# Performance work log

Hardware: AMD Instinct MI355X
Metric: run time of the kernel (lower is better)

## Reference

```python
import jax, jax.numpy as jnp
import numpy as np

H_DIM = 1024


def setup_inputs() -> dict:
    key = jax.random.key(0)
    k1, k2, k3, k4 = jax.random.split(key, 4)
    B, S, H = 8, 2048, H_DIM
    scale = 1.0 / np.sqrt(H)
    x = jax.random.normal(k1, (B, S, H), dtype=jnp.float32)
    attention_mask = jnp.ones((B, S), dtype=jnp.int32)
    wq = jax.random.normal(k2, (H, H), dtype=jnp.float32) * scale
    wk = jax.random.normal(k3, (H, H), dtype=jnp.float32) * scale
    wv = jax.random.normal(k4, (H, H), dtype=jnp.float32) * scale
    return {"x": x, "attention_mask": attention_mask, "wq": wq, "wk": wk, "wv": wv}


def reference(x, attention_mask, wq, wk, wv):
    # x: [B,S,H]; torch Linear(no bias): y = x @ W.T
    B, S, H = x.shape
    q = jnp.einsum('bsh,oh->bso', x, wq)
    k = jnp.einsum('bsh,oh->bso', x, wk)
    v = jnp.einsum('bsh,oh->bso', x, wv)
    qk = jnp.einsum('bqh,bkh->bqk', q, k) / jnp.sqrt(jnp.asarray(H, jnp.float32))
    # causal: mask positions where key index > query index (strict upper triangle)
    causal = jnp.triu(jnp.ones((S, S), dtype=bool), k=1)  # [S,S]
    m = attention_mask.astype(bool)                        # [B,S]
    allowed = m[:, None, :] & m[:, :, None]                # d & e: key-valid AND query-valid
    condition = causal[None, :, :] | jnp.logical_not(allowed)
    qk = jnp.where(condition, -jnp.inf, qk)
    att = jax.nn.softmax(qk, axis=-1)
    att = jnp.where(jnp.isnan(att), 0.0, att)  # fully-masked rows -> 0
    return jnp.einsum('bqk,bkh->bqh', att, v)
```

## Files before the change

kernel.cpp:

```cpp
#include <hip/hip_runtime.h>
#include <stdint.h>

typedef unsigned short u16;
typedef __bf16 bf16x8 __attribute__((ext_vector_type(8)));
typedef float f32x4 __attribute__((ext_vector_type(4)));
typedef u16 ushort8 __attribute__((ext_vector_type(8)));

#define SB 8
#define SS 2048
#define SH 1024
#define MTOT (SB*SS)
#define LOG2E 1.44269504088896f
#define SEXP (1.44269504088896f/32.f)

typedef __attribute__((address_space(3))) void lds_void;
typedef __attribute__((address_space(1))) const void gbl_void;

__device__ __forceinline__ float bf2f(u16 v) {
    union { unsigned int u; float f; } x; x.u = ((unsigned int)v) << 16; return x.f;
}
__device__ __forceinline__ u16 f2bf(float f) {
    unsigned int u = __builtin_bit_cast(unsigned int, f);
    u += 0x7fffu + ((u >> 16) & 1u);
    return (u16)(u >> 16);
}

__global__ void cvt_all(const float* __restrict__ x,  const float* __restrict__ wq,
                        const float* __restrict__ wk, const float* __restrict__ wv,
                        u16* __restrict__ xb, u16* __restrict__ wb) {
    const int NX = MTOT * SH / 8, NW = SH * SH / 8;
    int i = blockIdx.x * 256 + threadIdx.x;
    const float* src; u16* dst; int off;
    if (i < NX)               { src = x;  dst = xb;                        off = i; }
    else if (i < NX + NW)     { src = wq; dst = wb;                        off = i - NX; }
    else if (i < NX + 2 * NW) { src = wk; dst = wb + (size_t)SH * SH;      off = i - NX - NW; }
    else                      { src = wv; dst = wb + (size_t)2 * SH * SH;  off = i - NX - 2 * NW; }
    const float4* p = (const float4*)(src + (size_t)off * 8);
    float4 a = p[0], b = p[1];
    ushort8 r;
    r[0] = f2bf(a.x); r[1] = f2bf(a.y); r[2] = f2bf(a.z); r[3] = f2bf(a.w);
    r[4] = f2bf(b.x); r[5] = f2bf(b.y); r[6] = f2bf(b.z); r[7] = f2bf(b.w);
    *(ushort8*)(dst + (size_t)off * 8) = r;
}

__device__ __forceinline__ void stage_tile(const u16* __restrict__ g, int ld,
                                           u16* lds, int w, int l) {
#pragma unroll
    for (int i = 0; i < 4; i++) {
        int chunk = i * 4 + w;
        int r = chunk * 8 + (l >> 3);
        int c = (l & 7) * 8;
        __builtin_amdgcn_global_load_lds(
            (gbl_void*)(g + (size_t)r * ld + c),
            (lds_void*)(lds + chunk * 512), 16, 0, 0);
    }
}

__device__ __forceinline__ void mfma_tile(const u16* As, const u16* Bs,
                                          f32x4 acc[4][4], int w, int l) {
    int wr = (w >> 1) * 64, wc = (w & 1) * 64;
    int lr = l & 15, lk = (l >> 4) * 8;
#pragma unroll
    for (int kk = 0; kk < 2; kk++) {
        bf16x8 af[4], bb[4];
#pragma unroll
        for (int m = 0; m < 4; m++)
            af[m] = *(const bf16x8*)(const void*)(As + (wr + m * 16 + lr) * 64 + kk * 32 + lk);
#pragma unroll
        for (int n = 0; n < 4; n++)
            bb[n] = *(const bf16x8*)(const void*)(Bs + (wc + n * 16 + lr) * 64 + kk * 32 + lk);
#pragma unroll
        for (int m = 0; m < 4; m++)
#pragma unroll
            for (int n = 0; n < 4; n++)
                acc[m][n] = __builtin_amdgcn_mfma_f32_16x16x32_bf16(af[m], bb[n], acc[m][n], 0, 0, 0);
    }
}

#define QNT 16

#define STAGE8(gbase, ld, bufidx, h, t) do {                                          \
    const u16* _g = (gbase) + ((size_t)((h)*128 + srow)) * (ld) + (size_t)(t)*64 + scol; \
    u16* _d = &lds4[bufidx][((h)*128 + (w << 3)) * 64];                               \
    __builtin_amdgcn_global_load_lds((gbl_void*)_g, (lds_void*)_d, 16, 0, 0);         \
    __builtin_amdgcn_global_load_lds((gbl_void*)(_g + (size_t)64*(ld)),               \
                                     (lds_void*)(_d + 64*64), 16, 0, 0);              \
} while (0)

#define LDA8(mf, kkv) (*(const bf16x8*)(const void*)(Ab + (wr + (mf)*16 + rrow)*64 + rk##kkv))
#define LDB8(nf, kkv) (*(const bf16x8*)(const void*)(Bb + (wc + (nf)*16 + rrow)*64 + rk##kkv))

#define MFMA_PAIR(mf, A0, A1)                                                          \
    acc[mf][0] = __builtin_amdgcn_mfma_f32_16x16x32_bf16(A0, b00, acc[mf][0], 0,0,0);  \
    acc[mf][0] = __builtin_amdgcn_mfma_f32_16x16x32_bf16(A1, b01, acc[mf][0], 0,0,0);  \
    acc[mf][1] = __builtin_amdgcn_mfma_f32_16x16x32_bf16(A0, b10, acc[mf][1], 0,0,0);  \
    acc[mf][1] = __builtin_amdgcn_mfma_f32_16x16x32_bf16(A1, b11, acc[mf][1], 0,0,0);  \
    acc[mf][2] = __builtin_amdgcn_mfma_f32_16x16x32_bf16(A0, b20, acc[mf][2], 0,0,0);  \
    acc[mf][2] = __builtin_amdgcn_mfma_f32_16x16x32_bf16(A1, b21, acc[mf][2], 0,0,0);  \
    acc[mf][3] = __builtin_amdgcn_mfma_f32_16x16x32_bf16(A0, b30, acc[mf][3], 0,0,0);  \
    acc[mf][3] = __builtin_amdgcn_mfma_f32_16x16x32_bf16(A1, b31, acc[mf][3], 0,0,0);

#define PH_BAR_MID()                       \
    __builtin_amdgcn_sched_barrier(0);     \
    __builtin_amdgcn_s_barrier();          \
    __builtin_amdgcn_sched_barrier(0);

#define PH_BAR_END()                       \
    __builtin_amdgcn_sched_barrier(0);     \
    __builtin_amdgcn_s_barrier();          \
    __builtin_amdgcn_sched_barrier(0);

__global__ __launch_bounds__(512, 2) void gemm_qkv8(
    const u16* __restrict__ X, const u16* __restrict__ W,
    u16* __restrict__ Q, u16* __restrict__ Kd, u16* __restrict__ Vd) {
    __shared__ u16 lds4[4][256 * 64];

    int tid = threadIdx.x, w = tid >> 6, l = tid & 63;
    int bid = blockIdx.x;
    int wg = (bid & 7) * 96 + (bid >> 3);
    int mt = wg / 12, nb = wg % 12;

    const u16* gA = X + (size_t)mt * 256 * SH;
    const u16* gB = W + (size_t)nb * 256 * SH;

    int srow = (w << 3) + (l >> 3);
    int scol = (((l & 7) ^ ((l >> 3) & 7)) << 3);
    int wr = (w >> 2) * 128, wc = (w & 3) * 64;
    int rrow = l & 15;
    int rk0 = (((l >> 4) ^ (l & 7)) << 3);
    int rk1 = (((4 + (l >> 4)) ^ (l & 7)) << 3);

    f32x4 acc[8][4];
#pragma unroll
    for (int m = 0; m < 8; m++)
#pragma unroll
        for (int n = 0; n < 4; n++) acc[m][n] = (f32x4){0.f, 0.f, 0.f, 0.f};

    STAGE8(gA, SH, 0, 0, 0); STAGE8(gA, SH, 0, 1, 0);
    STAGE8(gB, SH, 2, 0, 0); STAGE8(gB, SH, 2, 1, 0);
    STAGE8(gB, SH, 3, 0, 1); STAGE8(gB, SH, 3, 1, 1);
    asm volatile("s_waitcnt vmcnt(4)" ::: "memory");
    __builtin_amdgcn_s_barrier();
    __builtin_amdgcn_sched_barrier(0);

    for (int t = 0; t < QNT; ++t) {
        const int p = t & 1;
        const u16* Ab = &lds4[p][0];
        const u16* Bb = &lds4[2 + p][0];

        bf16x8 b00 = LDB8(0, 0), b01 = LDB8(0, 1), b10 = LDB8(1, 0), b11 = LDB8(1, 1);
        bf16x8 b20 = LDB8(2, 0), b21 = LDB8(2, 1), b30 = LDB8(3, 0), b31 = LDB8(3, 1);
        {
            bf16x8 a00 = LDA8(0, 0), a01 = LDA8(0, 1), a10 = LDA8(1, 0), a11 = LDA8(1, 1);
            bf16x8 a20 = LDA8(2, 0), a21 = LDA8(2, 1), a30 = LDA8(3, 0), a31 = LDA8(3, 1);
            if (t + 1 < QNT) { STAGE8(gA, SH, (t + 1) & 1, 0, t + 1); STAGE8(gA, SH, (t + 1) & 1, 1, t + 1); }
            PH_BAR_MID();
            __builtin_amdgcn_s_setprio(1);
            MFMA_PAIR(0, a00, a01);
            MFMA_PAIR(1, a10, a11);
            MFMA_PAIR(2, a20, a21);
            MFMA_PAIR(3, a30, a31);
            __builtin_amdgcn_s_setprio(0);
            PH_BAR_END();
        }
        {
            bf16x8 a00 = LDA8(4, 0), a01 = LDA8(4, 1), a10 = LDA8(5, 0), a11 = LDA8(5, 1);
            bf16x8 a20 = LDA8(6, 0), a21 = LDA8(6, 1), a30 = LDA8(7, 0), a31 = LDA8(7, 1);
            if (t + 2 < QNT) { STAGE8(gB, SH, 2 + (t & 1), 0, t + 2); STAGE8(gB, SH, 2 + (t & 1), 1, t + 2); }
            if (t + 2 < QNT)      asm volatile("s_waitcnt vmcnt(4)" ::: "memory");
            else if (t + 1 < QNT) asm volatile("s_waitcnt vmcnt(0)" ::: "memory");
            PH_BAR_MID();
            __builtin_amdgcn_s_setprio(1);
            MFMA_PAIR(4, a00, a01);
            MFMA_PAIR(5, a10, a11);
            MFMA_PAIR(6, a20, a21);
            MFMA_PAIR(7, a30, a31);
            __builtin_amdgcn_s_setprio(0);
            PH_BAR_END();
        }
    }

    u16* outp = (nb < 4 ? Q : (nb < 8 ? Kd : Vd));
    size_t colb = (size_t)(nb & 3) * 256;
    int g = l >> 4, c = l & 15;
    u16* S = &lds4[0][0];
    __syncthreads();
#pragma unroll
    for (int pass = 0; pass < 2; ++pass) {
        if ((w >> 2) == pass) {
#pragma unroll
            for (int mf = 0; mf < 8; mf++)
#pragma unroll
                for (int j = 0; j < 4; j++) {
                    int rl = mf * 16 + g * 4 + j;
#pragma unroll
                    for (int nf = 0; nf < 4; nf++)
                        S[rl * 264 + wc + nf * 16 + c] = f2bf(acc[mf][nf][j]);
                }
        }
        __syncthreads();
#pragma unroll
        for (int q8 = 0; q8 < 8; ++q8) {
            int idx = q8 * 4096 + tid * 8;
            int row = idx >> 8;
            int colu = idx & 255;
            *(ushort8*)(outp + ((size_t)(mt * 256 + pass * 128 + row)) * SH + colb + colu)
                = *(const ushort8*)(S + row * 264 + colu);
        }
        __syncthreads();
    }
}

__global__ void transpose_v(const u16* __restrict__ V, u16* __restrict__ Vt) {
    __shared__ u16 t[64][80];
    int s0 = blockIdx.x * 64, o0 = blockIdx.y * 64, b = blockIdx.z;
    const u16* src = V + (size_t)b * SS * SH;
    u16* dst = Vt + (size_t)b * SH * SS;
    int tid = threadIdx.x;
#pragma unroll
    for (int it = 0; it < 2; it++) {
        int idx = it * 256 + tid;
        int r = idx >> 3, gq = idx & 7;
        *(ushort8*)&t[r][gq * 8] = *(const ushort8*)&src[(size_t)(s0 + r) * SH + o0 + gq * 8];
    }
    __syncthreads();
#pragma unroll
    for (int it = 0; it < 2; it++) {
        int idx = it * 256 + tid;
        int rr = idx >> 3, cc = idx & 7;
        ushort8 v;
#pragma unroll
        for (int e = 0; e < 8; e++) v[e] = t[cc * 8 + e][rr];
        *(ushort8*)&dst[(size_t)(o0 + rr) * SS + s0 + cc * 8] = v;
    }
}

__global__ __launch_bounds__(256, 2) void gemm_scores(
    const u16* __restrict__ Q, const u16* __restrict__ K,
    u16* __restrict__ P, float* __restrict__ lb,
    const int* __restrict__ amask) {
    __shared__ u16 As[128 * 64];
    __shared__ u16 Bs[128 * 64];
    int tid = threadIdx.x, w = tid >> 6, l = tid & 63;
    int x = blockIdx.x;
    int wk_ = (x & 7) * 136 + (x >> 3);
    int b = wk_ / 136, t = wk_ % 136;
    int qt = (int)((sqrtf(8.f * (float)t + 1.f) - 1.f) * 0.5f);
    while ((qt + 1) * (qt + 2) / 2 <= t) qt++;
    while (qt * (qt + 1) / 2 > t) qt--;
    int kt = t - qt * (qt + 1) / 2;
    const u16* A = Q + ((size_t)b * SS + (size_t)qt * 128) * SH;
    const u16* Bt = K + ((size_t)b * SS + (size_t)kt * 128) * SH;
    f32x4 acc[4][4];
#pragma unroll
    for (int m = 0; m < 4; m++)
#pragma unroll
        for (int n = 0; n < 4; n++) acc[m][n] = (f32x4){0.f, 0.f, 0.f, 0.f};
    for (int k0 = 0; k0 < SH; k0 += 64) {
        stage_tile(A + k0, SH, As, w, l);
        stage_tile(Bt + k0, SH, Bs, w, l);
        __syncthreads();
        mfma_tile(As, Bs, acc, w, l);
        __syncthreads();
    }
    int wr = (w >> 1) * 64, wc = (w & 1) * 64, g = l >> 4, c = l & 15;
    int q0 = qt * 128 + wr;
    int k0w = kt * 128 + wc;
    int cglob = kt * 2 + (w & 1);
    u16* Pb = P + (size_t)b * SS * SS;
    float* lbb = lb + (size_t)b * SS * 32;
    int kg[4], kv[4];
#pragma unroll
    for (int n = 0; n < 4; n++) { kg[n] = k0w + n * 16 + c; kv[n] = amask[b * SS + kg[n]]; }
#pragma unroll
    for (int m = 0; m < 4; m++) {
#pragma unroll
        for (int j = 0; j < 4; j++) {
            int qg = q0 + m * 16 + g * 4 + j;
            float sv[4]; float ls = 0.f;
#pragma unroll
            for (int n = 0; n < 4; n++) {
                bool ok = (kg[n] <= qg) && (kv[n] != 0);
                float p = ok ? exp2f(acc[m][n][j] * SEXP) : 0.f;
                sv[n] = p; ls += p;
            }
#pragma unroll
            for (int d = 1; d < 16; d <<= 1) ls += __shfl_xor(ls, d, 64);
            size_t prow = (size_t)qg * SS;
#pragma unroll
            for (int n = 0; n < 4; n++) Pb[prow + kg[n]] = f2bf(sv[n]);
            if (c == 0) lbb[(size_t)qg * 32 + cglob] = ls;
        }
    }
}

__global__ void combine_inv(const float* __restrict__ lb,
                            float* __restrict__ sb, const int* __restrict__ amask) {
    int row = blockIdx.x * 4 + (threadIdx.x >> 6);
    int l = threadIdx.x & 63;
    int b = row >> 11, q = row & 2047;
    int cmax = q >> 6;
    float L = (l < 32 && l <= cmax) ? lb[(size_t)row * 32 + l] : 0.f;
#pragma unroll
    for (int d = 1; d < 64; d <<= 1) L += __shfl_xor(L, d, 64);
    if (l == 0) {
        int qv = amask[b * SS + q];
        sb[row] = (qv != 0 && L > 0.f) ? 1.0f / L : 0.f;
    }
}

__global__ __launch_bounds__(256, 2) void gemm_pv(
    const u16* __restrict__ P, const u16* __restrict__ Vt,
    const float* __restrict__ sb, float* __restrict__ Out) {
    __shared__ u16 As[128 * 64];
    __shared__ u16 Bs[128 * 64];
    int tid = threadIdx.x, w = tid >> 6, l = tid & 63;
    int x = blockIdx.x;
    int wk_ = (x & 7) * 128 + (x >> 3);
    int b = wk_ >> 7;
    int r7 = wk_ & 127;
    int qt = 15 - (r7 >> 3), nt = r7 & 7;
    const u16* Ab = P + (size_t)b * SS * SS + (size_t)qt * 128 * SS;
    const u16* Bt = Vt + (size_t)b * SH * SS + (size_t)nt * 128 * SS;
    int ksize = (qt + 1) * 128;
    f32x4 acc[4][4];
#pragma unroll
    for (int m = 0; m < 4; m++)
#pragma unroll
        for (int n = 0; n < 4; n++) acc[m][n] = (f32x4){0.f, 0.f, 0.f, 0.f};
    for (int k0 = 0; k0 < ksize; k0 += 64) {
        stage_tile(Ab + k0, SS, As, w, l);
        stage_tile(Bt + k0, SS, Bs, w, l);
        __syncthreads();
        mfma_tile(As, Bs, acc, w, l);
        __syncthreads();
    }
    const float* sbq = sb + (size_t)b * SS + (size_t)qt * 128;
    float* out = Out + ((size_t)b * SS + (size_t)qt * 128) * SH + nt * 128;
    int wr = (w >> 1) * 64, wc = (w & 1) * 64, g = l >> 4, c = l & 15;
#pragma unroll
    for (int m = 0; m < 4; m++)
#pragma unroll
        for (int j = 0; j < 4; j++) {
            int row = wr + m * 16 + g * 4 + j;
            float scl = sbq[row];
            size_t ro = (size_t)row * SH;
#pragma unroll
            for (int n = 0; n < 4; n++)
                out[ro + wc + n * 16 + c] = acc[m][n][j] * scl;
        }
}

extern "C" void kernel_launch(void* const* d_in, const int* in_sizes, int n_in,
                              void* d_out, int out_size, void* d_ws, size_t ws_size,
                              hipStream_t stream) {
    const float* x = (const float*)d_in[0];
    const int* amask = (const int*)d_in[1];
    const float* wq = (const float*)d_in[2];
    const float* wk = (const float*)d_in[3];
    const float* wv = (const float*)d_in[4];
    float* out = (float*)d_out;

    const size_t SZQ = (size_t)MTOT * SH * 2;
    const size_t SZSTAT = (size_t)MTOT * 32 * 4;
    char* ws = (char*)d_ws;
    u16* Q   = (u16*)(ws);
    u16* Kb  = (u16*)(ws + SZQ);
    u16* V   = (u16*)(ws + 2 * SZQ);
    u16* Vt  = (u16*)(ws + 3 * SZQ);
    float* lb = (float*)(ws + 4 * SZQ);
    float* sb = (float*)(ws + 4 * SZQ + SZSTAT);
    u16* P   = (u16*)(ws + 4 * SZQ + 3 * SZSTAT);
    u16* xb  = P;
    u16* wb  = P + (size_t)MTOT * SH;

    cvt_all<<<9728, 256, 0, stream>>>(x, wq, wk, wv, xb, wb);

    gemm_qkv8<<<768, 512, 0, stream>>>(xb, wb, Q, Kb, V);
    transpose_v<<<dim3(32, 16, 8), 256, 0, stream>>>(V, Vt);
    gemm_scores<<<1088, 256, 0, stream>>>(Q, Kb, P, lb, amask);
    combine_inv<<<4096, 256, 0, stream>>>(lb, sb, amask);
    gemm_pv<<<1024, 256, 0, stream>>>(P, Vt, sb, out);
}
```

Before: 348.3 us.

## Fuse V transpose into QKV GEMM epilogue and split main loop into quarter phases

```diff
diff --git a/kernel.cpp b/kernel.cpp
--- a/kernel.cpp
+++ b/kernel.cpp
@@ -10,7 +10,6 @@
 #define SS 2048
 #define SH 1024
 #define MTOT (SB*SS)
-#define LOG2E 1.44269504088896f
 #define SEXP (1.44269504088896f/32.f)
 
 typedef __attribute__((address_space(3))) void lds_void;
@@ -112,7 +111,7 @@
 
 __global__ __launch_bounds__(512, 2) void gemm_qkv8(
     const u16* __restrict__ X, const u16* __restrict__ W,
-    u16* __restrict__ Q, u16* __restrict__ Kd, u16* __restrict__ Vd) {
+    u16* __restrict__ Q, u16* __restrict__ Kd, u16* __restrict__ Vt) {
     __shared__ u16 lds4[4][256 * 64];
 
     int tid = threadIdx.x, w = tid >> 6, l = tid & 63;
@@ -152,38 +151,56 @@
         bf16x8 b20 = LDB8(2, 0), b21 = LDB8(2, 1), b30 = LDB8(3, 0), b31 = LDB8(3, 1);
         {
             bf16x8 a00 = LDA8(0, 0), a01 = LDA8(0, 1), a10 = LDA8(1, 0), a11 = LDA8(1, 1);
-            bf16x8 a20 = LDA8(2, 0), a21 = LDA8(2, 1), a30 = LDA8(3, 0), a31 = LDA8(3, 1);
-            if (t + 1 < QNT) { STAGE8(gA, SH, (t + 1) & 1, 0, t + 1); STAGE8(gA, SH, (t + 1) & 1, 1, t + 1); }
+            if (t + 1 < QNT) STAGE8(gA, SH, (t + 1) & 1, 0, t + 1);
             PH_BAR_MID();
             __builtin_amdgcn_s_setprio(1);
             MFMA_PAIR(0, a00, a01);
             MFMA_PAIR(1, a10, a11);
-            MFMA_PAIR(2, a20, a21);
-            MFMA_PAIR(3, a30, a31);
             __builtin_amdgcn_s_setprio(0);
             PH_BAR_END();
         }
         {
+            bf16x8 a00 = LDA8(2, 0), a01 = LDA8(2, 1), a10 = LDA8(3, 0), a11 = LDA8(3, 1);
+            if (t + 1 < QNT) STAGE8(gA, SH, (t + 1) & 1, 1, t + 1);
+            PH_BAR_MID();
+            __builtin_amdgcn_s_setprio(1);
+            MFMA_PAIR(2, a00, a01);
+            MFMA_PAIR(3, a10, a11);
+            __builtin_amdgcn_s_setprio(0);
+            PH_BAR_END();
+        }
+        {
             bf16x8 a00 = LDA8(4, 0), a01 = LDA8(4, 1), a10 = LDA8(5, 0), a11 = LDA8(5, 1);
-            bf16x8 a20 = LDA8(6, 0), a21 = LDA8(6, 1), a30 = LDA8(7, 0), a31 = LDA8(7, 1);
-            if (t + 2 < QNT) { STAGE8(gB, SH, 2 + (t & 1), 0, t + 2); STAGE8(gB, SH, 2 + (t & 1), 1, t + 2); }
+            if (t + 2 < QNT) STAGE8(gB, SH, 2 + (t & 1), 0, t + 2);
+            PH_BAR_MID();
+            __builtin_amdgcn_s_setprio(1);
+            MFMA_PAIR(4, a00, a01);
+            MFMA_PAIR(5, a10, a11);
+            __builtin_amdgcn_s_setprio(0);
+            PH_BAR_END();
+        }
+        {
+            bf16x8 a00 = LDA8(6, 0), a01 = LDA8(6, 1), a10 = LDA8(7, 0), a11 = LDA8(7, 1);
+            if (t + 2 < QNT) STAGE8(gB, SH, 2 + (t & 1), 1, t + 2);
             if (t + 2 < QNT)      asm volatile("s_waitcnt vmcnt(4)" ::: "memory");
             else if (t + 1 < QNT) asm volatile("s_waitcnt vmcnt(0)" ::: "memory");
             PH_BAR_MID();
             __builtin_amdgcn_s_setprio(1);
-            MFMA_PAIR(4, a00, a01);
-            MFMA_PAIR(5, a10, a11);
-            MFMA_PAIR(6, a20, a21);
-            MFMA_PAIR(7, a30, a31);
+            MFMA_PAIR(6, a00, a01);
+            MFMA_PAIR(7, a10, a11);
             __builtin_amdgcn_s_setprio(0);
             PH_BAR_END();
         }
     }
 
-    u16* outp = (nb < 4 ? Q : (nb < 8 ? Kd : Vd));
+    bool isV = (nb >= 8);
+    u16* outp = (nb < 4 ? Q : Kd);
     size_t colb = (size_t)(nb & 3) * 256;
     int g = l >> 4, c = l & 15;
     u16* S = &lds4[0][0];
+    int bb_ = mt >> 3;
+    u16* vtb = Vt + (size_t)bb_ * SH * SS;
+    int sloc = (mt & 7) * 256;
     __syncthreads();
 #pragma unroll
     for (int pass = 0; pass < 2; ++pass) {
@@ -199,39 +216,28 @@
                 }
         }
         __syncthreads();
-#pragma unroll
-        for (int q8 = 0; q8 < 8; ++q8) {
-            int idx = q8 * 4096 + tid * 8;
-            int row = idx >> 8;
-            int colu = idx & 255;
-            *(ushort8*)(outp + ((size_t)(mt * 256 + pass * 128 + row)) * SH + colb + colu)
-                = *(const ushort8*)(S + row * 264 + colu);
-        }
-        __syncthreads();
-    }
-}
-
-__global__ void transpose_v(const u16* __restrict__ V, u16* __restrict__ Vt) {
-    __shared__ u16 t[64][80];
-    int s0 = blockIdx.x * 64, o0 = blockIdx.y * 64, b = blockIdx.z;
-    const u16* src = V + (size_t)b * SS * SH;
-    u16* dst = Vt + (size_t)b * SH * SS;
-    int tid = threadIdx.x;
-#pragma unroll
-    for (int it = 0; it < 2; it++) {
-        int idx = it * 256 + tid;
-        int r = idx >> 3, gq = idx & 7;
-        *(ushort8*)&t[r][gq * 8] = *(const ushort8*)&src[(size_t)(s0 + r) * SH + o0 + gq * 8];
-    }
-    __syncthreads();
-#pragma unroll
-    for (int it = 0; it < 2; it++) {
-        int idx = it * 256 + tid;
-        int rr = idx >> 3, cc = idx & 7;
-        ushort8 v;
-#pragma unroll
-        for (int e = 0; e < 8; e++) v[e] = t[cc * 8 + e][rr];
-        *(ushort8*)&dst[(size_t)(o0 + rr) * SS + s0 + cc * 8] = v;
+        if (!isV) {
+#pragma unroll
+            for (int q8 = 0; q8 < 8; ++q8) {
+                int idx = q8 * 4096 + tid * 8;
+                int row = idx >> 8;
+                int colu = idx & 255;
+                *(ushort8*)(outp + ((size_t)(mt * 256 + pass * 128 + row)) * SH + colb + colu)
+                    = *(const ushort8*)(S + row * 264 + colu);
+            }
+        } else {
+            int sbase = sloc + pass * 128;
+#pragma unroll
+            for (int it = 0; it < 8; ++it) {
+                int task = it * 512 + tid;
+                int o = task & 255, sg = task >> 8;
+                ushort8 v;
+#pragma unroll
+                for (int e = 0; e < 8; e++) v[e] = S[(sg * 8 + e) * 264 + o];
+                *(ushort8*)(vtb + (size_t)(colb + o) * SS + sbase + sg * 8) = v;
+            }
+        }
+        __syncthreads();
     }
 }
 
@@ -296,17 +302,13 @@
 
 __global__ void combine_inv(const float* __restrict__ lb,
                             float* __restrict__ sb, const int* __restrict__ amask) {
-    int row = blockIdx.x * 4 + (threadIdx.x >> 6);
-    int l = threadIdx.x & 63;
+    int row = blockIdx.x * 256 + threadIdx.x;
     int b = row >> 11, q = row & 2047;
     int cmax = q >> 6;
-    float L = (l < 32 && l <= cmax) ? lb[(size_t)row * 32 + l] : 0.f;
-#pragma unroll
-    for (int d = 1; d < 64; d <<= 1) L += __shfl_xor(L, d, 64);
-    if (l == 0) {
-        int qv = amask[b * SS + q];
-        sb[row] = (qv != 0 && L > 0.f) ? 1.0f / L : 0.f;
-    }
+    const float* p = lb + (size_t)row * 32;
+    float L = 0.f;
+    for (int i = 0; i <= cmax; i++) L += p[i];
+    sb[row] = (amask[b * SS + q] != 0 && L > 0.f) ? 1.0f / L : 0.f;
 }
 
 __global__ __launch_bounds__(256, 2) void gemm_pv(
@@ -366,8 +368,7 @@
     char* ws = (char*)d_ws;
     u16* Q   = (u16*)(ws);
     u16* Kb  = (u16*)(ws + SZQ);
-    u16* V   = (u16*)(ws + 2 * SZQ);
-    u16* Vt  = (u16*)(ws + 3 * SZQ);
+    u16* Vt  = (u16*)(ws + 2 * SZQ);
     float* lb = (float*)(ws + 4 * SZQ);
     float* sb = (float*)(ws + 4 * SZQ + SZSTAT);
     u16* P   = (u16*)(ws + 4 * SZQ + 3 * SZSTAT);
@@ -376,9 +377,8 @@
 
     cvt_all<<<9728, 256, 0, stream>>>(x, wq, wk, wv, xb, wb);
 
-    gemm_qkv8<<<768, 512, 0, stream>>>(xb, wb, Q, Kb, V);
-    transpose_v<<<dim3(32, 16, 8), 256, 0, stream>>>(V, Vt);
+    gemm_qkv8<<<768, 512, 0, stream>>>(xb, wb, Q, Kb, Vt);
     gemm_scores<<<1088, 256, 0, stream>>>(Q, Kb, P, lb, amask);
-    combine_inv<<<4096, 256, 0, stream>>>(lb, sb, amask);
+    combine_inv<<<64, 256, 0, stream>>>(lb, sb, amask);
     gemm_pv<<<1024, 256, 0, stream>>>(P, Vt, sb, out);
 }
```

Result: faster. 341.1 us (-2.1%).
